# Kernel optimization log

Hardware: AMD Instinct MI355X
Metric: run time of the kernel (lower is better)

## Reference

```python
import jax, jax.numpy as jnp
import numpy as np

N_NODES = 10000
N_EDGES = 160000
IN_DIM = 512
HID = 128
HEADS = 8
EMB = 256
NEG_SLOPE = 0.2  # PyG GATConv default


def setup_inputs() -> dict:
    key = jax.random.key(0)
    ks = jax.random.split(key, 12)
    x = jax.random.normal(ks[0], (N_NODES, IN_DIM), dtype=jnp.float32)
    edge_index = jax.random.randint(ks[1], (2, N_EDGES), 0, N_NODES, dtype=jnp.int64)
    s1 = 1.0 / np.sqrt(IN_DIM)
    s2 = 1.0 / np.sqrt(HEADS * HID)
    W1 = jax.random.normal(ks[2], (IN_DIM, HEADS * HID), dtype=jnp.float32) * s1
    a_src1 = jax.random.normal(ks[3], (HEADS, HID), dtype=jnp.float32) * s2
    a_dst1 = jax.random.normal(ks[4], (HEADS, HID), dtype=jnp.float32) * s2
    b1 = jnp.zeros((HEADS * HID,), dtype=jnp.float32)
    W2 = jax.random.normal(ks[5], (HEADS * HID, EMB), dtype=jnp.float32) * s2
    a_src2 = jax.random.normal(ks[6], (1, EMB), dtype=jnp.float32) * (1.0 / np.sqrt(EMB))
    a_dst2 = jax.random.normal(ks[7], (1, EMB), dtype=jnp.float32) * (1.0 / np.sqrt(EMB))
    b2 = jnp.zeros((EMB,), dtype=jnp.float32)
    return {"x": x, "edge_index": edge_index, "W1": W1, "a_src1": a_src1,
            "a_dst1": a_dst1, "b1": b1, "W2": W2, "a_src2": a_src2,
            "a_dst2": a_dst2, "b2": b2}


def gat_layer(h_in, src, dst, W, a_src, a_dst, b, concat, num_nodes):
    """PyG-style GATConv (eval mode, self-loops already in src/dst)."""
    H, C = a_src.shape
    h = (h_in @ W).reshape(num_nodes, H, C)            # [N, H, C]
    alpha_src = jnp.einsum('nhc,hc->nh', h, a_src)      # [N, H]
    alpha_dst = jnp.einsum('nhc,hc->nh', h, a_dst)      # [N, H]
    e = jax.nn.leaky_relu(alpha_src[src] + alpha_dst[dst], NEG_SLOPE)  # [E, H]
    # segment softmax over incoming edges of each destination node
    m = jax.ops.segment_max(e, dst, num_segments=num_nodes)            # [N, H]
    ex = jnp.exp(e - m[dst])
    denom = jax.ops.segment_sum(ex, dst, num_segments=num_nodes)       # [N, H]
    alpha = ex / denom[dst]                                            # [E, H]
    out = jax.ops.segment_sum(h[src] * alpha[:, :, None], dst,
                              num_segments=num_nodes)                  # [N, H, C]
    out = out.reshape(num_nodes, H * C) if concat else out.mean(axis=1)
    return out + b


def reference(x, edge_index, W1, a_src1, a_dst1, b1, W2, a_src2, a_dst2, b2):
    N = x.shape[0]
    loops = jnp.arange(N, dtype=edge_index.dtype)
    src = jnp.concatenate([edge_index[0], loops])
    dst = jnp.concatenate([edge_index[1], loops])
    h = gat_layer(x, src, dst, W1, a_src1, a_dst1, b1, concat=True, num_nodes=N)
    h = jax.nn.elu(h)  # dropout inactive in eval mode
    out = gat_layer(h, src, dst, W2, a_src2, a_dst2, b2, concat=False, num_nodes=N)
    return out
```

## Files before the change

kernel.cpp:

```cpp
#include <hip/hip_runtime.h>
#include <hip/hip_bf16.h>

typedef __attribute__((ext_vector_type(8))) short short8;
typedef __attribute__((ext_vector_type(4))) float floatx4;
typedef __attribute__((ext_vector_type(4))) unsigned short ushort4v;
typedef __attribute__((ext_vector_type(8))) unsigned short ushort8v;

#define NN 10000
#define E0 160000
#define ETOT (E0 + NN)
#define IN_DIM 512
#define HID1 1024
#define EMB 256
#define MPAD 10112
#define NX (NN * IN_DIM)
#define NW1 (IN_DIM * HID1)
#define NW2 (HID1 * EMB)

__device__ __forceinline__ float bf2f(unsigned short u) {
    unsigned v = ((unsigned)u) << 16;
    float f;
    __builtin_memcpy(&f, &v, 4);
    return f;
}
__device__ __forceinline__ unsigned short f2bf(float f) {
    unsigned u;
    __builtin_memcpy(&u, &f, 4);
    unsigned lsb = (u >> 16) & 1;
    u += 0x7fff + lsb;
    return (unsigned short)(u >> 16);
}
__device__ __forceinline__ float loadf(const void* p, size_t i, int isf32) {
    if (isf32) return ((const float*)p)[i];
    return bf2f(((const unsigned short*)p)[i]);
}

__global__ void zero_kernel(int* p, int n) {
    int i = blockIdx.x * 256 + threadIdx.x;
    if (i < n) p[i] = 0;
}

__global__ __launch_bounds__(1024) void fdetect_kernel(const unsigned* xw, int* isf32) {
    __shared__ int cnt[1024];
    int t = threadIdx.x;
    int c = 0;
    #pragma unroll
    for (int j = 0; j < 4; ++j) {
        unsigned w = xw[t * 4 + j];
        int ex = (w >> 7) & 0xFF;
        if (ex >= 110 && ex <= 135) c++;
    }
    cnt[t] = c;
    __syncthreads();
    for (int off = 512; off > 0; off >>= 1) {
        if (t < off) cnt[t] += cnt[t + off];
        __syncthreads();
    }
    if (t == 0) *isf32 = (cnt[0] < 2048) ? 1 : 0;
}

__global__ void detect_kernel(const int* ei32, int* flag) {
    int i = blockIdx.x * 256 + threadIdx.x;
    int v = 0;
    int idx = 2 * i + 1;
    if (idx < 2 * E0) v = ei32[idx];
    unsigned long long any = __ballot(v != 0);
    if (any && (threadIdx.x & 63) == 0) atomicOr(flag, 1);
}

__device__ __forceinline__ int load_edge(const void* ei, long long idx, int m32) {
    if (m32) return ((const int*)ei)[idx];
    return (int)(((const long long*)ei)[idx]);
}

__global__ void count_kernel(const void* ei, const int* flag, int* counts) {
    int e = blockIdx.x * 256 + threadIdx.x;
    if (e < E0) {
        int m32 = (*flag != 0);
        int d = load_edge(ei, (long long)E0 + e, m32);
        if (d >= 0 && d < NN) atomicAdd(&counts[d], 1);
    }
}

__global__ __launch_bounds__(1024) void scan_kernel(const int* counts, int* offsets, int* cursor) {
    __shared__ int part[1024];
    int t = threadIdx.x;
    int base = t * 10;
    int local[10];
    int s = 0;
    for (int j = 0; j < 10; ++j) {
        int idx = base + j;
        int v = (idx < NN) ? (counts[idx] + 1) : 0;
        local[j] = v; s += v;
    }
    part[t] = s;
    __syncthreads();
    for (int off = 1; off < 1024; off <<= 1) {
        int v = (t >= off) ? part[t - off] : 0;
        __syncthreads();
        part[t] += v;
        __syncthreads();
    }
    int run = (t == 0) ? 0 : part[t - 1];
    for (int j = 0; j < 10; ++j) {
        int idx = base + j;
        if (idx < NN) { offsets[idx] = run; cursor[idx] = run; run += local[j]; }
    }
    if (t == 1023) offsets[NN] = part[1023];
}

__global__ void scatter_kernel(const void* ei, const int* flag, int* cursor, int* csr_src) {
    int e = blockIdx.x * 256 + threadIdx.x;
    if (e >= ETOT) return;
    int m32 = (*flag != 0);
    int s, d;
    if (e < E0) { s = load_edge(ei, e, m32); d = load_edge(ei, (long long)E0 + e, m32); }
    else { s = d = e - E0; }
    if (s < 0) s = 0; if (s >= NN) s = NN - 1;
    if (d < 0) d = 0; if (d >= NN) d = NN - 1;
    int pos = atomicAdd(&cursor[d], 1);
    if (pos >= 0 && pos < ETOT) csr_src[pos] = s;
}

__global__ void convall_kernel(const void* x, const void* W1, const void* W2,
                               unsigned short* xb, unsigned short* W1t, unsigned short* W2t,
                               const int* isf32)
{
    int i = blockIdx.x * 256 + threadIdx.x;
    int f = *isf32;
    if (i < NX) { xb[i] = f2bf(loadf(x, i, f)); return; }
    i -= NX;
    if (i < NW1) {
        int r = i / HID1, c = i % HID1;
        W1t[(size_t)c * IN_DIM + r] = f2bf(loadf(W1, i, f));
        return;
    }
    i -= NW1;
    if (i < NW2) {
        int r = i / EMB, c = i % EMB;
        W2t[(size_t)c * HID1 + r] = f2bf(loadf(W2, i, f));
    }
}

template<bool OUTBF16>
__global__ __launch_bounds__(256) void gemm_tile(
    const unsigned short* __restrict__ A,
    const unsigned short* __restrict__ Bt,
    void* __restrict__ Cv,
    int N, int K)
{
    __shared__ unsigned short As[128 * 32];
    __shared__ unsigned short Bs[128 * 32];
    int t = threadIdx.x;
    int wave = t >> 6;
    int lane = t & 63;
    int quad = lane >> 4;
    int l16  = lane & 15;
    int mq = wave & 1, nq = wave >> 1;
    size_t mblk = (size_t)blockIdx.x * 128;
    size_t nblk = (size_t)blockIdx.y * 128;

    floatx4 acc[4][4];
    #pragma unroll
    for (int i = 0; i < 4; ++i)
        #pragma unroll
        for (int j = 0; j < 4; ++j)
            acc[i][j] = (floatx4){0.f, 0.f, 0.f, 0.f};

    const unsigned short* Abase = A + mblk * K;
    const unsigned short* Bbase = Bt + nblk * K;

    for (int kk = 0; kk < K; kk += 32) {
        __syncthreads();
        #pragma unroll
        for (int j = 0; j < 2; ++j) {
            int chunk = (wave << 7) + (j << 6) + lane;
            int r  = chunk >> 2;
            int cs = (chunk & 3) ^ (r & 3);
            const unsigned short* ga = Abase + (size_t)r * K + kk + cs * 8;
            const unsigned short* gb = Bbase + (size_t)r * K + kk + cs * 8;
            __builtin_amdgcn_global_load_lds(
                (const __attribute__((address_space(1))) void*)ga,
                (__attribute__((address_space(3))) void*)(As + (size_t)((wave << 7) + (j << 6)) * 8),
                16, 0, 0);
            __builtin_amdgcn_global_load_lds(
                (const __attribute__((address_space(1))) void*)gb,
                (__attribute__((address_space(3))) void*)(Bs + (size_t)((wave << 7) + (j << 6)) * 8),
                16, 0, 0);
        }
        __syncthreads();

        short8 af[4], bf[4];
        #pragma unroll
        for (int i = 0; i < 4; ++i) {
            int ar = mq * 64 + i * 16 + l16;
            int br = nq * 64 + i * 16 + l16;
            af[i] = *(const short8*)(const void*)(As + ar * 32 + (quad ^ (ar & 3)) * 8);
            bf[i] = *(const short8*)(const void*)(Bs + br * 32 + (quad ^ (br & 3)) * 8);
        }
        #pragma unroll
        for (int i = 0; i < 4; ++i)
            #pragma unroll
            for (int j = 0; j < 4; ++j)
                acc[i][j] = __builtin_amdgcn_mfma_f32_16x16x32_bf16(af[i], bf[j], acc[i][j], 0, 0, 0);
    }

    size_t crow0 = mblk + mq * 64 + quad * 4;
    size_t ccol0 = nblk + nq * 64 + l16;
    #pragma unroll
    for (int i = 0; i < 4; ++i) {
        #pragma unroll
        for (int r = 0; r < 4; ++r) {
            size_t row = crow0 + i * 16 + r;
            size_t b = row * N + ccol0;
            #pragma unroll
            for (int j = 0; j < 4; ++j) {
                if (OUTBF16) ((unsigned short*)Cv)[b + j * 16] = f2bf(acc[i][j][r]);
                else         ((float*)Cv)[b + j * 16] = acc[i][j][r];
            }
        }
    }
}

__global__ __launch_bounds__(256) void alpha1_kernel(
    const unsigned short* __restrict__ h1,
    const void* __restrict__ a_src, const void* __restrict__ a_dst,
    const int* __restrict__ isf32,
    float* __restrict__ as1, float* __restrict__ ad1)
{
    int n = blockIdx.x, t = threadIdx.x;
    int f = *isf32;
    ushort4v hv = *(const ushort4v*)(const void*)(h1 + (size_t)n * HID1 + t * 4);
    float ps = 0.f, pd = 0.f;
    #pragma unroll
    for (int i = 0; i < 4; ++i) {
        float h = bf2f(hv[i]);
        ps += h * loadf(a_src, t * 4 + i, f);
        pd += h * loadf(a_dst, t * 4 + i, f);
    }
    __shared__ float rs[256], rdm[256];
    rs[t] = ps; rdm[t] = pd;
    __syncthreads();
    for (int off = 16; off > 0; off >>= 1) {
        if ((t & 31) < off) { rs[t] += rs[t + off]; rdm[t] += rdm[t + off]; }
        __syncthreads();
    }
    if ((t & 31) == 0) {
        int h = t >> 5;
        as1[n * 8 + h] = rs[t];
        ad1[n * 8 + h] = rdm[t];
    }
}

__global__ __launch_bounds__(256) void agg1_kernel(
    const unsigned short* __restrict__ h1, const int* __restrict__ offsets,
    const int* __restrict__ csr_src, const float* __restrict__ as1,
    const float* __restrict__ ad1, const void* __restrict__ b1,
    const int* __restrict__ isf32,
    unsigned short* __restrict__ hmid)
{
    int n = blockIdx.x, t = threadIdx.x;
    int f = *isf32;
    int beg = offsets[n], end = offsets[n + 1];
    if (beg < 0) beg = 0; if (end > ETOT) end = ETOT;
    int g = t >> 7;
    int u = t & 127;
    int c0 = u * 8;
    int hc = u >> 4;
    float ad = ad1[n * 8 + hc];

    float den = 0.f;
    float acc[8];
    #pragma unroll
    for (int j = 0; j < 8; ++j) acc[j] = 0.f;

    int i = beg + g;
    for (; i + 6 < end; i += 8) {
        int s0 = csr_src[i];     s0 &= 0x7fffffff; if (s0 >= NN) s0 = 0;
        int s1 = csr_src[i + 2]; s1 &= 0x7fffffff; if (s1 >= NN) s1 = 0;
        int s2 = csr_src[i + 4]; s2 &= 0x7fffffff; if (s2 >= NN) s2 = 0;
        int s3 = csr_src[i + 6]; s3 &= 0x7fffffff; if (s3 >= NN) s3 = 0;
        ushort8v hv0 = *(const ushort8v*)(const void*)(h1 + (size_t)s0 * HID1 + c0);
        ushort8v hv1 = *(const ushort8v*)(const void*)(h1 + (size_t)s1 * HID1 + c0);
        ushort8v hv2 = *(const ushort8v*)(const void*)(h1 + (size_t)s2 * HID1 + c0);
        ushort8v hv3 = *(const ushort8v*)(const void*)(h1 + (size_t)s3 * HID1 + c0);
        float e0 = as1[s0 * 8 + hc] + ad;
        float e1 = as1[s1 * 8 + hc] + ad;
        float e2 = as1[s2 * 8 + hc] + ad;
        float e3 = as1[s3 * 8 + hc] + ad;
        e0 = e0 > 0.f ? e0 : 0.2f * e0;
        e1 = e1 > 0.f ? e1 : 0.2f * e1;
        e2 = e2 > 0.f ? e2 : 0.2f * e2;
        e3 = e3 > 0.f ? e3 : 0.2f * e3;
        float w0 = __expf(e0), w1 = __expf(e1), w2 = __expf(e2), w3 = __expf(e3);
        den += (w0 + w1) + (w2 + w3);
        #pragma unroll
        for (int j = 0; j < 8; ++j)
            acc[j] += (bf2f(hv0[j]) * w0 + bf2f(hv1[j]) * w1)
                    + (bf2f(hv2[j]) * w2 + bf2f(hv3[j]) * w3);
    }
    for (; i + 2 < end; i += 4) {
        int s0 = csr_src[i];     s0 &= 0x7fffffff; if (s0 >= NN) s0 = 0;
        int s1 = csr_src[i + 2]; s1 &= 0x7fffffff; if (s1 >= NN) s1 = 0;
        ushort8v hv0 = *(const ushort8v*)(const void*)(h1 + (size_t)s0 * HID1 + c0);
        ushort8v hv1 = *(const ushort8v*)(const void*)(h1 + (size_t)s1 * HID1 + c0);
        float e0 = as1[s0 * 8 + hc] + ad;
        float e1 = as1[s1 * 8 + hc] + ad;
        e0 = e0 > 0.f ? e0 : 0.2f * e0;
        e1 = e1 > 0.f ? e1 : 0.2f * e1;
        float w0 = __expf(e0), w1 = __expf(e1);
        den += w0 + w1;
        #pragma unroll
        for (int j = 0; j < 8; ++j)
            acc[j] += bf2f(hv0[j]) * w0 + bf2f(hv1[j]) * w1;
    }
    if (i < end) {
        int s0 = csr_src[i]; s0 &= 0x7fffffff; if (s0 >= NN) s0 = 0;
        ushort8v hv0 = *(const ushort8v*)(const void*)(h1 + (size_t)s0 * HID1 + c0);
        float e0 = as1[s0 * 8 + hc] + ad;
        e0 = e0 > 0.f ? e0 : 0.2f * e0;
        float w0 = __expf(e0);
        den += w0;
        #pragma unroll
        for (int j = 0; j < 8; ++j) acc[j] += bf2f(hv0[j]) * w0;
    }

    __shared__ float accsh[128][9];
    __shared__ float densh[128];
    if (g == 1) {
        #pragma unroll
        for (int j = 0; j < 8; ++j) accsh[u][j] = acc[j];
        densh[u] = den;
    }
    __syncthreads();
    if (g == 0) {
        den += densh[u];
        float rden = 1.0f / fmaxf(den, 1e-30f);
        ushort8v outw;
        #pragma unroll
        for (int j = 0; j < 8; ++j) {
            float v = (acc[j] + accsh[u][j]) * rden + loadf(b1, c0 + j, f);
            v = v > 0.f ? v : (__expf(v) - 1.0f);
            outw[j] = f2bf(v);
        }
        *(ushort8v*)(void*)(hmid + (size_t)n * HID1 + c0) = outw;
    }
}

__global__ __launch_bounds__(256) void alpha2_kernel(
    const unsigned short* __restrict__ h2,
    const void* __restrict__ a_src2, const void* __restrict__ a_dst2,
    const int* __restrict__ isf32,
    float* __restrict__ as2, float* __restrict__ ad2)
{
    int n = blockIdx.x, t = threadIdx.x;
    int f = *isf32;
    float v = bf2f(h2[(size_t)n * EMB + t]);
    float ps = v * loadf(a_src2, t, f);
    float pd = v * loadf(a_dst2, t, f);
    __shared__ float rs[256], rdm[256];
    rs[t] = ps; rdm[t] = pd;
    __syncthreads();
    for (int off = 128; off > 0; off >>= 1) {
        if (t < off) { rs[t] += rs[t + off]; rdm[t] += rdm[t + off]; }
        __syncthreads();
    }
    if (t == 0) { as2[n] = rs[0]; ad2[n] = rdm[0]; }
}

__global__ __launch_bounds__(256) void agg2_kernel(
    const unsigned short* __restrict__ h2, const int* __restrict__ offsets,
    const int* __restrict__ csr_src, const float* __restrict__ as2,
    const float* __restrict__ ad2, const void* __restrict__ b2,
    const int* __restrict__ isf32,
    float* __restrict__ out)
{
    int n = blockIdx.x, t = threadIdx.x;
    int f = *isf32;
    int beg = offsets[n], end = offsets[n + 1];
    if (beg < 0) beg = 0; if (end > ETOT) end = ETOT;
    int g = t >> 6;
    int u = t & 63;
    int c0 = u * 4;
    float adn = ad2[n];

    float den = 0.f;
    float acc[4];
    #pragma unroll
    for (int j = 0; j < 4; ++j) acc[j] = 0.f;

    int i = beg + g;
    for (; i + 12 < end; i += 16) {
        int s0 = csr_src[i];      s0 &= 0x7fffffff; if (s0 >= NN) s0 = 0;
        int s1 = csr_src[i + 4];  s1 &= 0x7fffffff; if (s1 >= NN) s1 = 0;
        int s2 = csr_src[i + 8];  s2 &= 0x7fffffff; if (s2 >= NN) s2 = 0;
        int s3 = csr_src[i + 12]; s3 &= 0x7fffffff; if (s3 >= NN) s3 = 0;
        ushort4v hv0 = *(const ushort4v*)(const void*)(h2 + (size_t)s0 * EMB + c0);
        ushort4v hv1 = *(const ushort4v*)(const void*)(h2 + (size_t)s1 * EMB + c0);
        ushort4v hv2 = *(const ushort4v*)(const void*)(h2 + (size_t)s2 * EMB + c0);
        ushort4v hv3 = *(const ushort4v*)(const void*)(h2 + (size_t)s3 * EMB + c0);
        float e0 = as2[s0] + adn;
        float e1 = as2[s1] + adn;
        float e2 = as2[s2] + adn;
        float e3 = as2[s3] + adn;
        e0 = e0 > 0.f ? e0 : 0.2f * e0;
        e1 = e1 > 0.f ? e1 : 0.2f * e1;
        e2 = e2 > 0.f ? e2 : 0.2f * e2;
        e3 = e3 > 0.f ? e3 : 0.2f * e3;
        float w0 = __expf(e0), w1 = __expf(e1), w2 = __expf(e2), w3 = __expf(e3);
        den += (w0 + w1) + (w2 + w3);
        #pragma unroll
        for (int j = 0; j < 4; ++j)
            acc[j] += (bf2f(hv0[j]) * w0 + bf2f(hv1[j]) * w1)
                    + (bf2f(hv2[j]) * w2 + bf2f(hv3[j]) * w3);
    }
    for (; i + 4 < end; i += 8) {
        int s0 = csr_src[i];     s0 &= 0x7fffffff; if (s0 >= NN) s0 = 0;
        int s1 = csr_src[i + 4]; s1 &= 0x7fffffff; if (s1 >= NN) s1 = 0;
        ushort4v hv0 = *(const ushort4v*)(const void*)(h2 + (size_t)s0 * EMB + c0);
        ushort4v hv1 = *(const ushort4v*)(const void*)(h2 + (size_t)s1 * EMB + c0);
        float e0 = as2[s0] + adn;
        float e1 = as2[s1] + adn;
        e0 = e0 > 0.f ? e0 : 0.2f * e0;
        e1 = e1 > 0.f ? e1 : 0.2f * e1;
        float w0 = __expf(e0), w1 = __expf(e1);
        den += w0 + w1;
        #pragma unroll
        for (int j = 0; j < 4; ++j)
            acc[j] += bf2f(hv0[j]) * w0 + bf2f(hv1[j]) * w1;
    }
    if (i < end) {
        int s0 = csr_src[i]; s0 &= 0x7fffffff; if (s0 >= NN) s0 = 0;
        ushort4v hv0 = *(const ushort4v*)(const void*)(h2 + (size_t)s0 * EMB + c0);
        float e0 = as2[s0] + adn;
        e0 = e0 > 0.f ? e0 : 0.2f * e0;
        float w0 = __expf(e0);
        den += w0;
        #pragma unroll
        for (int j = 0; j < 4; ++j) acc[j] += bf2f(hv0[j]) * w0;
    }

    __shared__ float accsh[4][64][5];
    __shared__ float densh[4][64];
    #pragma unroll
    for (int j = 0; j < 4; ++j) accsh[g][u][j] = acc[j];
    densh[g][u] = den;
    __syncthreads();
    if (g == 0) {
        float dtot = densh[0][u] + densh[1][u] + densh[2][u] + densh[3][u];
        float rden = 1.0f / fmaxf(dtot, 1e-30f);
        floatx4 o;
        #pragma unroll
        for (int j = 0; j < 4; ++j) {
            float v = (accsh[0][u][j] + accsh[1][u][j] + accsh[2][u][j] + accsh[3][u][j]) * rden;
            o[j] = v + loadf(b2, c0 + j, f);
        }
        *(floatx4*)(void*)(out + (size_t)n * EMB + c0) = o;
    }
}

extern "C" void kernel_launch(void* const* d_in, const int* in_sizes, int n_in,
                              void* d_out, int out_size, void* d_ws, size_t ws_size,
                              hipStream_t stream)
{
    const void* x      = d_in[0];
    const void* edge   = d_in[1];
    const void* W1     = d_in[2];
    const void* a_src1 = d_in[3];
    const void* a_dst1 = d_in[4];
    const void* b1     = d_in[5];
    const void* W2     = d_in[6];
    const void* a_src2 = d_in[7];
    const void* a_dst2 = d_in[8];
    const void* b2     = d_in[9];
    float* out = (float*)d_out;

    char* ws = (char*)d_ws;
    size_t off = 0;
    auto alloc = [&](size_t bytes) -> void* {
        void* p = ws + off;
        off += (bytes + 255) & ~(size_t)255;
        return p;
    };
    int*            counts = (int*)alloc((NN + 2) * 4);
    int*            offs   = (int*)alloc((NN + 1) * 4);
    int*            cursor = (int*)alloc(NN * 4);
    int*            csr    = (int*)alloc((size_t)ETOT * 4);
    float*          as1    = (float*)alloc((size_t)NN * 8 * 4);
    float*          ad1    = (float*)alloc((size_t)NN * 8 * 4);
    float*          as2    = (float*)alloc((size_t)NN * 4);
    float*          ad2    = (float*)alloc((size_t)NN * 4);
    unsigned short* xb     = (unsigned short*)alloc((size_t)MPAD * IN_DIM * 2);
    unsigned short* W1t    = (unsigned short*)alloc((size_t)IN_DIM * HID1 * 2);
    unsigned short* W2t    = (unsigned short*)alloc((size_t)HID1 * EMB * 2);
    unsigned short* h1b    = (unsigned short*)alloc((size_t)MPAD * HID1 * 2);
    unsigned short* hmid   = (unsigned short*)alloc((size_t)MPAD * HID1 * 2);
    unsigned short* h2b    = (unsigned short*)alloc((size_t)MPAD * EMB * 2);
    int* eflag = counts + NN;
    int* isf32 = counts + NN + 1;

    zero_kernel<<<(NN + 2 + 255) / 256, 256, 0, stream>>>(counts, NN + 2);
    fdetect_kernel<<<1, 1024, 0, stream>>>((const unsigned*)x, isf32);
    detect_kernel<<<(E0 + 255) / 256, 256, 0, stream>>>((const int*)edge, eflag);

    count_kernel<<<(E0 + 255) / 256, 256, 0, stream>>>(edge, eflag, counts);
    scan_kernel<<<1, 1024, 0, stream>>>(counts, offs, cursor);
    scatter_kernel<<<(ETOT + 255) / 256, 256, 0, stream>>>(edge, eflag, cursor, csr);

    convall_kernel<<<(NX + NW1 + NW2 + 255) / 256, 256, 0, stream>>>(
        x, W1, W2, xb, W1t, W2t, isf32);

    dim3 g1(MPAD / 128, HID1 / 128);
    gemm_tile<true><<<g1, 256, 0, stream>>>(xb, W1t, h1b, HID1, IN_DIM);

    alpha1_kernel<<<NN, 256, 0, stream>>>(h1b, a_src1, a_dst1, isf32, as1, ad1);
    agg1_kernel<<<NN, 256, 0, stream>>>(h1b, offs, csr, as1, ad1, b1, isf32, hmid);

    dim3 g2(MPAD / 128, EMB / 128);
    gemm_tile<true><<<g2, 256, 0, stream>>>(hmid, W2t, h2b, EMB, HID1);

    alpha2_kernel<<<NN, 256, 0, stream>>>(h2b, a_src2, a_dst2, isf32, as2, ad2);
    agg2_kernel<<<NN, 256, 0, stream>>>(h2b, offs, csr, as2, ad2, b2, isf32, out);
}
```

Measured before the change: 300.0 us.

## Merge detection kernels, use shuffle scans/reductions, widen agg1 per-thread columns

Merges the two input-format detection kernels into one launch, so the pipeline has one fewer kernel. The scan and alpha1 reductions now use wavefront shuffles instead of shared-memory loops with many barriers. agg1 now gives each thread 16 columns through two 128-bit loads and splits edges across four groups instead of two. Together these aim to cut launch overhead, barrier cost and gather latency, at the cost of more registers in agg1 and a larger shared-memory combine.

```diff
diff --git a/kernel.cpp b/kernel.cpp
--- a/kernel.cpp
+++ b/kernel.cpp
@@ -5,6 +5,8 @@
 typedef __attribute__((ext_vector_type(4))) float floatx4;
 typedef __attribute__((ext_vector_type(4))) unsigned short ushort4v;
 typedef __attribute__((ext_vector_type(8))) unsigned short ushort8v;
+typedef __attribute__((ext_vector_type(2))) unsigned int uint2v;
+typedef __attribute__((ext_vector_type(4))) unsigned int uint4v;
 
 #define NN 10000
 #define E0 160000
@@ -16,11 +18,22 @@
 #define NX (NN * IN_DIM)
 #define NW1 (IN_DIM * HID1)
 #define NW2 (HID1 * EMB)
+#define DETB 625
 
 __device__ __forceinline__ float bf2f(unsigned short u) {
     unsigned v = ((unsigned)u) << 16;
     float f;
     __builtin_memcpy(&f, &v, 4);
+    return f;
+}
+__device__ __forceinline__ float bflo(unsigned v) {
+    unsigned x = v << 16;
+    float f; __builtin_memcpy(&f, &x, 4);
+    return f;
+}
+__device__ __forceinline__ float bfhi(unsigned v) {
+    unsigned x = v & 0xffff0000u;
+    float f; __builtin_memcpy(&f, &x, 4);
     return f;
 }
 __device__ __forceinline__ unsigned short f2bf(float f) {
@@ -30,42 +43,47 @@
     u += 0x7fff + lsb;
     return (unsigned short)(u >> 16);
 }
+__device__ __forceinline__ unsigned packbf(float lo, float hi) {
+    return (unsigned)f2bf(lo) | ((unsigned)f2bf(hi) << 16);
+}
 __device__ __forceinline__ float loadf(const void* p, size_t i, int isf32) {
     if (isf32) return ((const float*)p)[i];
     return bf2f(((const unsigned short*)p)[i]);
 }
+__device__ __forceinline__ float lrelu(float e) { return e > 0.f ? e : 0.2f * e; }
 
 __global__ void zero_kernel(int* p, int n) {
     int i = blockIdx.x * 256 + threadIdx.x;
     if (i < n) p[i] = 0;
 }
 
-__global__ __launch_bounds__(1024) void fdetect_kernel(const unsigned* xw, int* isf32) {
-    __shared__ int cnt[1024];
+__global__ __launch_bounds__(256) void probe_kernel(const int* ei32, const unsigned* xw,
+                                                    int* eflag, int* isf32) {
     int t = threadIdx.x;
-    int c = 0;
-    #pragma unroll
-    for (int j = 0; j < 4; ++j) {
-        unsigned w = xw[t * 4 + j];
-        int ex = (w >> 7) & 0xFF;
-        if (ex >= 110 && ex <= 135) c++;
-    }
-    cnt[t] = c;
-    __syncthreads();
-    for (int off = 512; off > 0; off >>= 1) {
-        if (t < off) cnt[t] += cnt[t + off];
+    if (blockIdx.x < DETB) {
+        int i = blockIdx.x * 256 + t;
+        int v = 0;
+        int idx = 2 * i + 1;
+        if (idx < 2 * E0) v = ei32[idx];
+        unsigned long long any = __ballot(v != 0);
+        if (any && (t & 63) == 0) atomicOr(eflag, 1);
+    } else {
+        __shared__ int cnt[256];
+        int c = 0;
+        #pragma unroll
+        for (int j = 0; j < 16; ++j) {
+            unsigned w = xw[t * 16 + j];
+            int ex = (w >> 7) & 0xFF;
+            if (ex >= 110 && ex <= 135) c++;
+        }
+        cnt[t] = c;
         __syncthreads();
-    }
-    if (t == 0) *isf32 = (cnt[0] < 2048) ? 1 : 0;
-}
-
-__global__ void detect_kernel(const int* ei32, int* flag) {
-    int i = blockIdx.x * 256 + threadIdx.x;
-    int v = 0;
-    int idx = 2 * i + 1;
-    if (idx < 2 * E0) v = ei32[idx];
-    unsigned long long any = __ballot(v != 0);
-    if (any && (threadIdx.x & 63) == 0) atomicOr(flag, 1);
+        for (int off = 128; off > 0; off >>= 1) {
+            if (t < off) cnt[t] += cnt[t + off];
+            __syncthreads();
+        }
+        if (t == 0) *isf32 = (cnt[0] < 2048) ? 1 : 0;
+    }
 }
 
 __device__ __forceinline__ int load_edge(const void* ei, long long idx, int m32) {
@@ -83,30 +101,44 @@
 }
 
 __global__ __launch_bounds__(1024) void scan_kernel(const int* counts, int* offsets, int* cursor) {
-    __shared__ int part[1024];
+    __shared__ int wsum[16];
     int t = threadIdx.x;
+    int lane = t & 63, wv = t >> 6;
     int base = t * 10;
     int local[10];
     int s = 0;
+    #pragma unroll
     for (int j = 0; j < 10; ++j) {
         int idx = base + j;
         int v = (idx < NN) ? (counts[idx] + 1) : 0;
         local[j] = v; s += v;
     }
-    part[t] = s;
+    int v = s;
+    #pragma unroll
+    for (int d = 1; d < 64; d <<= 1) {
+        int o = __shfl_up(v, d, 64);
+        if (lane >= d) v += o;
+    }
+    if (lane == 63) wsum[wv] = v;
     __syncthreads();
-    for (int off = 1; off < 1024; off <<= 1) {
-        int v = (t >= off) ? part[t - off] : 0;
-        __syncthreads();
-        part[t] += v;
-        __syncthreads();
-    }
-    int run = (t == 0) ? 0 : part[t - 1];
+    if (t < 16) {
+        int w = wsum[t];
+        #pragma unroll
+        for (int d = 1; d < 16; d <<= 1) {
+            int o = __shfl_up(w, d, 16);
+            if (t >= d) w += o;
+        }
+        wsum[t] = w;
+    }
+    __syncthreads();
+    int woff = (wv == 0) ? 0 : wsum[wv - 1];
+    int run = woff + v - s;
+    #pragma unroll
     for (int j = 0; j < 10; ++j) {
         int idx = base + j;
         if (idx < NN) { offsets[idx] = run; cursor[idx] = run; run += local[j]; }
     }
-    if (t == 1023) offsets[NN] = part[1023];
+    if (t == 1023) offsets[NN] = wsum[15];
 }
 
 __global__ void scatter_kernel(const void* ei, const int* flag, int* cursor, int* csr_src) {
@@ -238,17 +270,15 @@
         ps += h * loadf(a_src, t * 4 + i, f);
         pd += h * loadf(a_dst, t * 4 + i, f);
     }
-    __shared__ float rs[256], rdm[256];
-    rs[t] = ps; rdm[t] = pd;
-    __syncthreads();
-    for (int off = 16; off > 0; off >>= 1) {
-        if ((t & 31) < off) { rs[t] += rs[t + off]; rdm[t] += rdm[t + off]; }
-        __syncthreads();
+    #pragma unroll
+    for (int off = 1; off < 32; off <<= 1) {
+        ps += __shfl_xor(ps, off, 64);
+        pd += __shfl_xor(pd, off, 64);
     }
     if ((t & 31) == 0) {
         int h = t >> 5;
-        as1[n * 8 + h] = rs[t];
-        ad1[n * 8 + h] = rdm[t];
+        as1[n * 8 + h] = ps;
+        ad1[n * 8 + h] = pd;
     }
 }
 
@@ -263,87 +293,105 @@
     int f = *isf32;
     int beg = offsets[n], end = offsets[n + 1];
     if (beg < 0) beg = 0; if (end > ETOT) end = ETOT;
-    int g = t >> 7;
-    int u = t & 127;
-    int c0 = u * 8;
-    int hc = u >> 4;
+    int g = t >> 6;
+    int u = t & 63;
+    int c0 = u * 16;
+    int hc = u >> 3;
     float ad = ad1[n * 8 + hc];
+    const unsigned* rb = (const unsigned*)h1 + u * 8;
 
     float den = 0.f;
-    float acc[8];
-    #pragma unroll
-    for (int j = 0; j < 8; ++j) acc[j] = 0.f;
+    float acc[16];
+    #pragma unroll
+    for (int j = 0; j < 16; ++j) acc[j] = 0.f;
 
     int i = beg + g;
-    for (; i + 6 < end; i += 8) {
+    for (; i + 12 < end; i += 16) {
+        int s0 = csr_src[i];      s0 &= 0x7fffffff; if (s0 >= NN) s0 = 0;
+        int s1 = csr_src[i + 4];  s1 &= 0x7fffffff; if (s1 >= NN) s1 = 0;
+        int s2 = csr_src[i + 8];  s2 &= 0x7fffffff; if (s2 >= NN) s2 = 0;
+        int s3 = csr_src[i + 12]; s3 &= 0x7fffffff; if (s3 >= NN) s3 = 0;
+        uint4v a0 = *(const uint4v*)(const void*)(rb + (size_t)s0 * 512);
+        uint4v b0 = *(const uint4v*)(const void*)(rb + (size_t)s0 * 512 + 4);
+        uint4v a1 = *(const uint4v*)(const void*)(rb + (size_t)s1 * 512);
+        uint4v b1v = *(const uint4v*)(const void*)(rb + (size_t)s1 * 512 + 4);
+        uint4v a2 = *(const uint4v*)(const void*)(rb + (size_t)s2 * 512);
+        uint4v b2v = *(const uint4v*)(const void*)(rb + (size_t)s2 * 512 + 4);
+        uint4v a3 = *(const uint4v*)(const void*)(rb + (size_t)s3 * 512);
+        uint4v b3v = *(const uint4v*)(const void*)(rb + (size_t)s3 * 512 + 4);
+        float w0 = __expf(lrelu(as1[s0 * 8 + hc] + ad));
+        float w1 = __expf(lrelu(as1[s1 * 8 + hc] + ad));
+        float w2 = __expf(lrelu(as1[s2 * 8 + hc] + ad));
+        float w3 = __expf(lrelu(as1[s3 * 8 + hc] + ad));
+        den += (w0 + w1) + (w2 + w3);
+        #pragma unroll
+        for (int q = 0; q < 4; ++q) {
+            acc[2 * q]      += (bflo(a0[q]) * w0 + bflo(a1[q]) * w1) + (bflo(a2[q]) * w2 + bflo(a3[q]) * w3);
+            acc[2 * q + 1]  += (bfhi(a0[q]) * w0 + bfhi(a1[q]) * w1) + (bfhi(a2[q]) * w2 + bfhi(a3[q]) * w3);
+            acc[8 + 2 * q]  += (bflo(b0[q]) * w0 + bflo(b1v[q]) * w1) + (bflo(b2v[q]) * w2 + bflo(b3v[q]) * w3);
+            acc[9 + 2 * q]  += (bfhi(b0[q]) * w0 + bfhi(b1v[q]) * w1) + (bfhi(b2v[q]) * w2 + bfhi(b3v[q]) * w3);
+        }
+    }
+    for (; i + 4 < end; i += 8) {
         int s0 = csr_src[i];     s0 &= 0x7fffffff; if (s0 >= NN) s0 = 0;
-        int s1 = csr_src[i + 2]; s1 &= 0x7fffffff; if (s1 >= NN) s1 = 0;
-        int s2 = csr_src[i + 4]; s2 &= 0x7fffffff; if (s2 >= NN) s2 = 0;
-        int s3 = csr_src[i + 6]; s3 &= 0x7fffffff; if (s3 >= NN) s3 = 0;
-        ushort8v hv0 = *(const ushort8v*)(const void*)(h1 + (size_t)s0 * HID1 + c0);
-        ushort8v hv1 = *(const ushort8v*)(const void*)(h1 + (size_t)s1 * HID1 + c0);
-        ushort8v hv2 = *(const ushort8v*)(const void*)(h1 + (size_t)s2 * HID1 + c0);
-        ushort8v hv3 = *(const ushort8v*)(const void*)(h1 + (size_t)s3 * HID1 + c0);
-        float e0 = as1[s0 * 8 + hc] + ad;
-        float e1 = as1[s1 * 8 + hc] + ad;
-        float e2 = as1[s2 * 8 + hc] + ad;
-        float e3 = as1[s3 * 8 + hc] + ad;
-        e0 = e0 > 0.f ? e0 : 0.2f * e0;
-        e1 = e1 > 0.f ? e1 : 0.2f * e1;
-        e2 = e2 > 0.f ? e2 : 0.2f * e2;
-        e3 = e3 > 0.f ? e3 : 0.2f * e3;
-        float w0 = __expf(e0), w1 = __expf(e1), w2 = __expf(e2), w3 = __expf(e3);
-        den += (w0 + w1) + (w2 + w3);
-        #pragma unroll
-        for (int j = 0; j < 8; ++j)
-            acc[j] += (bf2f(hv0[j]) * w0 + bf2f(hv1[j]) * w1)
-                    + (bf2f(hv2[j]) * w2 + bf2f(hv3[j]) * w3);
-    }
-    for (; i + 2 < end; i += 4) {
-        int s0 = csr_src[i];     s0 &= 0x7fffffff; if (s0 >= NN) s0 = 0;
-        int s1 = csr_src[i + 2]; s1 &= 0x7fffffff; if (s1 >= NN) s1 = 0;
-        ushort8v hv0 = *(const ushort8v*)(const void*)(h1 + (size_t)s0 * HID1 + c0);
-        ushort8v hv1 = *(const ushort8v*)(const void*)(h1 + (size_t)s1 * HID1 + c0);
-        float e0 = as1[s0 * 8 + hc] + ad;
-        float e1 = as1[s1 * 8 + hc] + ad;
-        e0 = e0 > 0.f ? e0 : 0.2f * e0;
-        e1 = e1 > 0.f ? e1 : 0.2f * e1;
-        float w0 = __expf(e0), w1 = __expf(e1);
+        int s1 = csr_src[i + 4]; s1 &= 0x7fffffff; if (s1 >= NN) s1 = 0;
+        uint4v a0 = *(const uint4v*)(const void*)(rb + (size_t)s0 * 512);
+        uint4v b0 = *(const uint4v*)(const void*)(rb + (size_t)s0 * 512 + 4);
+        uint4v a1 = *(const uint4v*)(const void*)(rb + (size_t)s1 * 512);
+        uint4v b1v = *(const uint4v*)(const void*)(rb + (size_t)s1 * 512 + 4);
+        float w0 = __expf(lrelu(as1[s0 * 8 + hc] + ad));
+        float w1 = __expf(lrelu(as1[s1 * 8 + hc] + ad));
         den += w0 + w1;
         #pragma unroll
-        for (int j = 0; j < 8; ++j)
-            acc[j] += bf2f(hv0[j]) * w0 + bf2f(hv1[j]) * w1;
+        for (int q = 0; q < 4; ++q) {
+            acc[2 * q]      += bflo(a0[q]) * w0 + bflo(a1[q]) * w1;
+            acc[2 * q + 1]  += bfhi(a0[q]) * w0 + bfhi(a1[q]) * w1;
+            acc[8 + 2 * q]  += bflo(b0[q]) * w0 + bflo(b1v[q]) * w1;
+            acc[9 + 2 * q]  += bfhi(b0[q]) * w0 + bfhi(b1v[q]) * w1;
+        }
     }
     if (i < end) {
         int s0 = csr_src[i]; s0 &= 0x7fffffff; if (s0 >= NN) s0 = 0;
-        ushort8v hv0 = *(const ushort8v*)(const void*)(h1 + (size_t)s0 * HID1 + c0);
-        float e0 = as1[s0 * 8 + hc] + ad;
-        e0 = e0 > 0.f ? e0 : 0.2f * e0;
-        float w0 = __expf(e0);
+        uint4v a0 = *(const uint4v*)(const void*)(rb + (size_t)s0 * 512);
+        uint4v b0 = *(const uint4v*)(const void*)(rb + (size_t)s0 * 512 + 4);
+        float w0 = __expf(lrelu(as1[s0 * 8 + hc] + ad));
         den += w0;
         #pragma unroll
-        for (int j = 0; j < 8; ++j) acc[j] += bf2f(hv0[j]) * w0;
-    }
-
-    __shared__ float accsh[128][9];
-    __shared__ float densh[128];
-    if (g == 1) {
-        #pragma unroll
-        for (int j = 0; j < 8; ++j) accsh[u][j] = acc[j];
-        densh[u] = den;
+        for (int q = 0; q < 4; ++q) {
+            acc[2 * q]      += bflo(a0[q]) * w0;
+            acc[2 * q + 1]  += bfhi(a0[q]) * w0;
+            acc[8 + 2 * q]  += bflo(b0[q]) * w0;
+            acc[9 + 2 * q]  += bfhi(b0[q]) * w0;
+        }
+    }
+
+    __shared__ float sh[3][64][17];
+    if (g) {
+        #pragma unroll
+        for (int j = 0; j < 16; ++j) sh[g - 1][u][j] = acc[j];
+        sh[g - 1][u][16] = den;
     }
     __syncthreads();
     if (g == 0) {
-        den += densh[u];
+        den += sh[0][u][16] + sh[1][u][16] + sh[2][u][16];
         float rden = 1.0f / fmaxf(den, 1e-30f);
-        ushort8v outw;
-        #pragma unroll
-        for (int j = 0; j < 8; ++j) {
-            float v = (acc[j] + accsh[u][j]) * rden + loadf(b1, c0 + j, f);
-            v = v > 0.f ? v : (__expf(v) - 1.0f);
-            outw[j] = f2bf(v);
-        }
-        *(ushort8v*)(void*)(hmid + (size_t)n * HID1 + c0) = outw;
+        uint4v oA, oB;
+        #pragma unroll
+        for (int q = 0; q < 4; ++q) {
+            float v0 = (acc[2 * q]     + sh[0][u][2 * q]     + sh[1][u][2 * q]     + sh[2][u][2 * q])     * rden + loadf(b1, c0 + 2 * q, f);
+            float v1 = (acc[2 * q + 1] + sh[0][u][2 * q + 1] + sh[1][u][2 * q + 1] + sh[2][u][2 * q + 1]) * rden + loadf(b1, c0 + 2 * q + 1, f);
+            v0 = v0 > 0.f ? v0 : (__expf(v0) - 1.0f);
+            v1 = v1 > 0.f ? v1 : (__expf(v1) - 1.0f);
+            oA[q] = packbf(v0, v1);
+            float u0 = (acc[8 + 2 * q] + sh[0][u][8 + 2 * q] + sh[1][u][8 + 2 * q] + sh[2][u][8 + 2 * q]) * rden + loadf(b1, c0 + 8 + 2 * q, f);
+            float u1 = (acc[9 + 2 * q] + sh[0][u][9 + 2 * q] + sh[1][u][9 + 2 * q] + sh[2][u][9 + 2 * q]) * rden + loadf(b1, c0 + 9 + 2 * q, f);
+            u0 = u0 > 0.f ? u0 : (__expf(u0) - 1.0f);
+            u1 = u1 > 0.f ? u1 : (__expf(u1) - 1.0f);
+            oB[q] = packbf(u0, u1);
+        }
+        unsigned* hw = (unsigned*)hmid;
+        *(uint4v*)(void*)(hw + (size_t)n * 512 + u * 8)     = oA;
+        *(uint4v*)(void*)(hw + (size_t)n * 512 + u * 8 + 4) = oB;
     }
 }
 
@@ -500,8 +548,7 @@
     int* isf32 = counts + NN + 1;
 
     zero_kernel<<<(NN + 2 + 255) / 256, 256, 0, stream>>>(counts, NN + 2);
-    fdetect_kernel<<<1, 1024, 0, stream>>>((const unsigned*)x, isf32);
-    detect_kernel<<<(E0 + 255) / 256, 256, 0, stream>>>((const int*)edge, eflag);
+    probe_kernel<<<DETB + 1, 256, 0, stream>>>((const int*)edge, (const unsigned*)x, eflag, isf32);
 
     count_kernel<<<(E0 + 255) / 256, 256, 0, stream>>>(edge, eflag, counts);
     scan_kernel<<<1, 1024, 0, stream>>>(counts, offs, cursor);
```

Result: no change. 301.4 us (+0.5%).
